# Kernel tuning notes

Measured on AMD Instinct MI355X. Metric: run time of the kernel, lower is better.

## Reference

```python
import jax, jax.numpy as jnp
import numpy as np

TAU = 2.0  # LIF membrane time constant (tau=2.0)
V_TH = 1.0  # spiking threshold (spikingjelly default)

@jax.custom_vjp
def spike(v):
    # Heaviside spike at v >= 0 (input is v - V_TH)
    return (v >= 0.0).astype(v.dtype)

def _spike_fwd(v):
    return spike(v), v

def _spike_bwd(v, g):
    # ATan surrogate gradient (spikingjelly default, alpha=2):
    # d/dv = alpha / (2 * (1 + (pi/2 * alpha * v)^2)) = 1 / (1 + (pi*v)^2)
    return (g / (1.0 + (jnp.pi * v) ** 2),)

spike.defvjp(_spike_fwd, _spike_bwd)

def lif_linear(x, w):
    """SpikLinearLayer: Linear (no bias) then multi-step LIF over leading T axis.
    x: [T, B, N, Din], w: [Dout, Din] -> spikes [T, B, N, Dout]
    LIF: v <- v + (y - v)/tau ; s = H(v - vth) ; hard reset v <- v*(1-s)
    """
    y = jnp.einsum('tbnd,ed->tbne', x, w)
    def step(v, yt):
        v = v + (yt - v) / TAU
        s = spike(v - V_TH)
        return v * (1.0 - s), s
    _, spikes = jax.lax.scan(step, jnp.zeros_like(y[0]), y)
    return spikes

def setup_inputs() -> dict:
    key = jax.random.key(0)
    k0, k1, k2, k3 = jax.random.split(key, 4)
    T, B, N, D, L = 4, 32, 1024, 256, 2
    x = jax.random.normal(k0, (T, B, N, D), dtype=jnp.float32)
    w_in = jax.random.normal(k1, (2 * D, D), dtype=jnp.float32) * 0.05
    w_hidden = jax.random.normal(k2, (L, 2 * D, 2 * D), dtype=jnp.float32) * 0.05
    w_out = jax.random.normal(k3, (D, 2 * D), dtype=jnp.float32) * 0.05
    return {"x": x, "w_in": w_in, "w_hidden": w_hidden, "w_out": w_out}

def reference(x, w_in, w_hidden, w_out):
    # TemporalBlock.forward
    h = lif_linear(x, w_in)                       # [T,B,N,2D]
    for l in range(w_hidden.shape[0]):
        h = h * (1.0 - lif_linear(h, w_hidden[l]))  # multiplicative spike gate
    return lif_linear(h, w_out)                   # [T,B,N,D]
```

## Files before the change

### kernel.cpp

```cpp
#include <hip/hip_runtime.h>
#include <stdint.h>

typedef __attribute__((ext_vector_type(8))) short short8;
typedef __attribute__((ext_vector_type(4))) float f32x4;

constexpr int T_ = 4;
constexpr int BNTOT = 32768;

__device__ __forceinline__ uint32_t bf1(float f) {
    uint32_t x = __builtin_bit_cast(uint32_t, f);
    return (x + 0x7FFFu + ((x >> 16) & 1u)) >> 16;
}
__device__ __forceinline__ uint32_t pk(float lo, float hi) {
    return bf1(lo) | (bf1(hi) << 16);
}

__global__ __launch_bounds__(256)
void cvt_tiled(const float* __restrict__ in, ushort* __restrict__ out) {
    const int g   = blockIdx.x * 256 + threadIdx.x;
    const int kg  = g & 31;
    const int r   = (g >> 5) & 15;
    const int bt  = g >> 9;
    const float* src = in + ((size_t)(bt * 16 + r)) * 256 + kg * 8;
    const float4 a = *(const float4*)src;
    const float4 b = *(const float4*)(src + 4);
    uint4 o;
    o.x = pk(a.x, a.y); o.y = pk(a.z, a.w);
    o.z = pk(b.x, b.y); o.w = pk(b.z, b.w);
    *(uint4*)(out + ((size_t)(bt * 32 + kg)) * 128 + r * 8) = o;
}

template <int MODE, int K, int NOUT>
__global__ __launch_bounds__(256, 3)
void lif_mfma(const ushort* __restrict__ A,
              const float* __restrict__ W,
              void* __restrict__ Out)
{
    __shared__ __align__(16) char smem[8192 + 32768];

    constexpr int NS = K / 32;
    constexpr int NCOLT = NOUT / 64;

    const int tid = threadIdx.x;
    const int l   = tid & 63;
    const int w   = tid >> 6;

    const int id  = blockIdx.x;
    const int xcd = id & 7;
    const int j_  = id >> 3;
    const int row0 = (xcd * 64 + j_ / NCOLT) * 64;
    const int col0 = (j_ % NCOLT) * 64;

    const int rby = (l & 15) * 64;
    const int gp  = ((l >> 4) ^ ((l >> 1) & 3)) << 4;

    const ushort* abase = A +
        ((size_t)(w * (BNTOT / 16) + (row0 >> 4)) * (K / 8) + (l >> 4)) * 128 +
        (l & 15) * 8;

    const int b_col = tid >> 2;
    const float* w_base = W + (size_t)(col0 + b_col) * K +
                          ((tid & 3) ^ ((tid >> 3) & 3)) * 8;
    const int bwo = b_col * 64 + (tid & 3) * 16;

    f32x4 acc[4][4];
#pragma unroll
    for (int m = 0; m < 4; ++m)
#pragma unroll
        for (int n = 0; n < 4; ++n) acc[m][n] = (f32x4)0.f;

    auto loadA = [&](int s, short8 af[4]) {
#pragma unroll
        for (int m = 0; m < 4; ++m)
            af[m] = *(const short8*)(abase + (size_t)m * (K * 16) + s * 512);
    };
    auto loadB = [&](int s, float4& f0, float4& f1) {
        const float* wp = w_base + s * 32;
        f0 = *(const float4*)wp;
        f1 = *(const float4*)(wp + 4);
    };
    auto writeB = [&](const float4& f0, const float4& f1, char* buf) {
        uint4 o;
        o.x = pk(f0.x, f0.y); o.y = pk(f0.z, f0.w);
        o.z = pk(f1.x, f1.y); o.w = pk(f1.z, f1.w);
        *(uint4*)(buf + bwo) = o;
    };
    auto compute = [&](const short8 af[4], const char* buf) {
        short8 bfr[4];
#pragma unroll
        for (int n = 0; n < 4; ++n)
            bfr[n] = *(const short8*)(buf + n * 1024 + rby + gp);
#pragma unroll
        for (int m = 0; m < 4; ++m)
#pragma unroll
            for (int n = 0; n < 4; ++n)
                acc[m][n] = __builtin_amdgcn_mfma_f32_16x16x32_bf16(
                    af[m], bfr[n], acc[m][n], 0, 0, 0);
    };

    char* const bs0 = smem;
    char* const bs1 = smem + 4096;

    short8 aEv[4], aOd[4];
    float4 bEv0, bEv1, bOd0, bOd1;

    loadA(0, aEv);
    loadB(0, bEv0, bEv1);
    writeB(bEv0, bEv1, bs0);
    asm volatile("s_waitcnt lgkmcnt(0)\n\ts_barrier" ::: "memory");

    for (int s = 0; s < NS; s += 2) {
        const int s1 = (s + 1 < NS) ? s + 1 : s;
        loadA(s1, aOd);
        loadB(s1, bOd0, bOd1);
        compute(aEv, bs0);
        writeB(bOd0, bOd1, bs1);
        asm volatile("s_waitcnt lgkmcnt(0)\n\ts_barrier" ::: "memory");

        const int s2 = (s + 2 < NS) ? s + 2 : s;
        loadA(s2, aEv);
        loadB(s2, bEv0, bEv1);
        compute(aOd, bs1);
        writeB(bEv0, bEv1, bs0);
        asm volatile("s_waitcnt lgkmcnt(0)\n\ts_barrier" ::: "memory");
    }

    float* Y = (float*)(smem + 8192);
#pragma unroll
    for (int half = 0; half < 2; ++half) {
#pragma unroll
        for (int nn = 0; nn < 2; ++nn) {
            const int n = half * 2 + nn;
#pragma unroll
            for (int m = 0; m < 4; ++m)
#pragma unroll
                for (int j = 0; j < 4; ++j) {
                    const int row = m * 16 + (l >> 4) * 4 + j;
                    const int cl  = nn * 16 + (l & 15);
                    const int colp = cl ^ (((row >> 2) & 1) << 4);
                    Y[w * 2048 + row * 32 + colp] = acc[m][n][j];
                }
        }
        __syncthreads();
#pragma unroll
        for (int u4 = 0; u4 < 4; ++u4) {
            const int u   = u4 * 256 + tid;
            const int row = u >> 4;
            const int cp  = (u & 15) * 2;
            const int colp = cp ^ (((row >> 2) & 1) << 4);
            float v0 = 0.f, v1 = 0.f;
#pragma unroll
            for (int t = 0; t < T_; ++t) {
                const float2 y = *(const float2*)&Y[t * 2048 + row * 32 + colp];
                v0 = 0.5f * (v0 + y.x);
                v1 = 0.5f * (v1 + y.y);
                const bool s0 = (v0 >= 1.f), s1 = (v1 >= 1.f);
                v0 = s0 ? 0.f : v0;
                v1 = s1 ? 0.f : v1;
                const int grow = row0 + row;
                const int c    = col0 + half * 32 + cp;
                if (MODE == 2) {
                    float2 o;
                    o.x = s0 ? 1.f : 0.f;
                    o.y = s1 ? 1.f : 0.f;
                    *(float2*)((float*)Out + ((size_t)(t * BNTOT + grow)) * NOUT + c) = o;
                } else {
                    const size_t tb = ((size_t)(t * (BNTOT / 16) + (grow >> 4)) *
                                       (NOUT / 8) + (c >> 3)) * 128 + (grow & 15) * 8 + (c & 7);
                    if (MODE == 0) {
                        uint32_t uo = (s0 ? 0x3F80u : 0u) | (s1 ? 0x3F800000u : 0u);
                        *(uint32_t*)((ushort*)Out + tb) = uo;
                    } else {
                        const uint32_t h = *(const uint32_t*)(A + tb);
                        const uint32_t msk = (s0 ? 0u : 0xFFFFu) | (s1 ? 0u : 0xFFFF0000u);
                        *(uint32_t*)((ushort*)Out + tb) = h & msk;
                    }
                }
            }
        }
        __syncthreads();
    }
}

extern "C" void kernel_launch(void* const* d_in, const int* in_sizes, int n_in,
                              void* d_out, int out_size, void* d_ws, size_t ws_size,
                              hipStream_t stream)
{
    const float* x     = (const float*)d_in[0];
    const float* w_in  = (const float*)d_in[1];
    const float* w_h   = (const float*)d_in[2];
    const float* w_out = (const float*)d_in[3];

    ushort* xbf = (ushort*)d_out;
    ushort* hA  = (ushort*)d_ws;
    ushort* hB  = (ushort*)d_out;
    float*  out = (float*)d_out;

    cvt_tiled<<<16384, 256, 0, stream>>>(x, xbf);

    lif_mfma<0, 256, 512><<<8 * 512, 256, 0, stream>>>(xbf, w_in, hA);
    lif_mfma<1, 512, 512><<<8 * 512, 256, 0, stream>>>(hA, w_h, hB);
    lif_mfma<1, 512, 512><<<8 * 512, 256, 0, stream>>>(hB, w_h + 512 * 512, hA);
    lif_mfma<2, 512, 256><<<4 * 512, 256, 0, stream>>>(hA, w_out, out);
}
```

Before: 409.5 us.

## Store spike activations as bytes, preload whole weight slab, fuse T into MFMA tile

Intermediate spike/gated activations are now stored as uint8 0/1 masks instead of bf16 and expanded to bf16 in registers with byte permutes and a multiply. This halves activation traffic between layers. The whole 64-column weight slab is converted into shared memory once per block, replacing the double-buffered per-step pipeline. Each wave now owns 16 rows across all four timesteps, so the LIF recurrence runs directly on accumulator registers without a shared-memory transpose. Risks: occupancy drops to 2 waves per SIMD and shared memory grows to 64KB for K=512. The byte-mask format is exact here only because the gated activations are always 0 or 1.

```diff
diff --git a/kernel.cpp b/kernel.cpp
--- a/kernel.cpp
+++ b/kernel.cpp
@@ -15,12 +15,21 @@
     return bf1(lo) | (bf1(hi) << 16);
 }
 
+__device__ __forceinline__ short8 expand8(uint2 r) {
+    uint4 o;
+    o.x = __builtin_amdgcn_perm(0u, r.x, 0x0C010C00u) * 0x3F80u;
+    o.y = __builtin_amdgcn_perm(0u, r.x, 0x0C030C02u) * 0x3F80u;
+    o.z = __builtin_amdgcn_perm(0u, r.y, 0x0C010C00u) * 0x3F80u;
+    o.w = __builtin_amdgcn_perm(0u, r.y, 0x0C030C02u) * 0x3F80u;
+    return __builtin_bit_cast(short8, o);
+}
+
 __global__ __launch_bounds__(256)
 void cvt_tiled(const float* __restrict__ in, ushort* __restrict__ out) {
-    const int g   = blockIdx.x * 256 + threadIdx.x;
-    const int kg  = g & 31;
-    const int r   = (g >> 5) & 15;
-    const int bt  = g >> 9;
+    const int g  = blockIdx.x * 256 + threadIdx.x;
+    const int kg = g & 31;
+    const int r  = (g >> 5) & 15;
+    const int bt = g >> 9;
     const float* src = in + ((size_t)(bt * 16 + r)) * 256 + kg * 8;
     const float4 a = *(const float4*)src;
     const float4 b = *(const float4*)(src + 4);
@@ -31,15 +40,15 @@
 }
 
 template <int MODE, int K, int NOUT>
-__global__ __launch_bounds__(256, 3)
-void lif_mfma(const ushort* __restrict__ A,
+__global__ __launch_bounds__(256, 2)
+void lif_mfma(const void* __restrict__ Av,
               const float* __restrict__ W,
               void* __restrict__ Out)
 {
-    __shared__ __align__(16) char smem[8192 + 32768];
-
     constexpr int NS = K / 32;
+    constexpr int KG = K / 8;
     constexpr int NCOLT = NOUT / 64;
+    __shared__ __align__(16) char smem[NS * 4096];
 
     const int tid = threadIdx.x;
     const int l   = tid & 63;
@@ -51,134 +60,128 @@
     const int row0 = (xcd * 64 + j_ / NCOLT) * 64;
     const int col0 = (j_ % NCOLT) * 64;
 
-    const int rby = (l & 15) * 64;
-    const int gp  = ((l >> 4) ^ ((l >> 1) & 3)) << 4;
-
-    const ushort* abase = A +
-        ((size_t)(w * (BNTOT / 16) + (row0 >> 4)) * (K / 8) + (l >> 4)) * 128 +
-        (l & 15) * 8;
-
-    const int b_col = tid >> 2;
-    const float* w_base = W + (size_t)(col0 + b_col) * K +
-                          ((tid & 3) ^ ((tid >> 3) & 3)) * 8;
-    const int bwo = b_col * 64 + (tid & 3) * 16;
-
-    f32x4 acc[4][4];
-#pragma unroll
-    for (int m = 0; m < 4; ++m)
-#pragma unroll
-        for (int n = 0; n < 4; ++n) acc[m][n] = (f32x4)0.f;
-
-    auto loadA = [&](int s, short8 af[4]) {
-#pragma unroll
-        for (int m = 0; m < 4; ++m)
-            af[m] = *(const short8*)(abase + (size_t)m * (K * 16) + s * 512);
-    };
-    auto loadB = [&](int s, float4& f0, float4& f1) {
-        const float* wp = w_base + s * 32;
-        f0 = *(const float4*)wp;
-        f1 = *(const float4*)(wp + 4);
-    };
-    auto writeB = [&](const float4& f0, const float4& f1, char* buf) {
-        uint4 o;
-        o.x = pk(f0.x, f0.y); o.y = pk(f0.z, f0.w);
-        o.z = pk(f1.x, f1.y); o.w = pk(f1.z, f1.w);
-        *(uint4*)(buf + bwo) = o;
-    };
-    auto compute = [&](const short8 af[4], const char* buf) {
+    {
+        constexpr int ITERS = 64 * KG / 256;
+#pragma unroll
+        for (int i = 0; i < ITERS; ++i) {
+            const int idx = i * 256 + tid;
+            const int c   = idx / KG;
+            const int kg  = idx % KG;
+            const float* wp = W + (size_t)(col0 + c) * K + kg * 8;
+            const float4 f0 = *(const float4*)wp;
+            const float4 f1 = *(const float4*)(wp + 4);
+            uint4 o;
+            o.x = pk(f0.x, f0.y); o.y = pk(f0.z, f0.w);
+            o.z = pk(f1.x, f1.y); o.w = pk(f1.z, f1.w);
+            const int s = kg >> 2, g = kg & 3;
+            *(uint4*)(smem + ((c >> 4) * NS + s) * 1024 + (c & 15) * 64 +
+                      ((g ^ ((c >> 1) & 3)) * 16)) = o;
+        }
+    }
+    __syncthreads();
+
+    const char* bbase = smem + (l & 15) * 64 + (((l >> 4) ^ ((l >> 1) & 3)) * 16);
+    const int rb = (row0 >> 4) + w;
+
+    f32x4 acc[T_][4];
+#pragma unroll
+    for (int t = 0; t < T_; ++t)
+#pragma unroll
+        for (int n = 0; n < 4; ++n) acc[t][n] = (f32x4)0.f;
+
+    size_t aunit[T_];
+#pragma unroll
+    for (int t = 0; t < T_; ++t)
+        aunit[t] = ((size_t)(t * (BNTOT / 16) + rb)) * KG + (l >> 4);
+
+    auto loadAb = [&](int s, short8 a[T_]) {
+#pragma unroll
+        for (int t = 0; t < T_; ++t)
+            a[t] = *(const short8*)((const ushort*)Av +
+                     (aunit[t] + s * 4) * 128 + (l & 15) * 8);
+    };
+    auto loadAu = [&](int s, uint2 a[T_]) {
+#pragma unroll
+        for (int t = 0; t < T_; ++t)
+            a[t] = *(const uint2*)((const uint8_t*)Av +
+                     (aunit[t] + s * 4) * 128 + (l & 15) * 8);
+    };
+    auto stepB = [&](const short8 a[T_], int s) {
         short8 bfr[4];
 #pragma unroll
         for (int n = 0; n < 4; ++n)
-            bfr[n] = *(const short8*)(buf + n * 1024 + rby + gp);
-#pragma unroll
-        for (int m = 0; m < 4; ++m)
+            bfr[n] = *(const short8*)(bbase + (n * NS + s) * 1024);
+#pragma unroll
+        for (int t = 0; t < T_; ++t)
 #pragma unroll
             for (int n = 0; n < 4; ++n)
-                acc[m][n] = __builtin_amdgcn_mfma_f32_16x16x32_bf16(
-                    af[m], bfr[n], acc[m][n], 0, 0, 0);
-    };
-
-    char* const bs0 = smem;
-    char* const bs1 = smem + 4096;
-
-    short8 aEv[4], aOd[4];
-    float4 bEv0, bEv1, bOd0, bOd1;
-
-    loadA(0, aEv);
-    loadB(0, bEv0, bEv1);
-    writeB(bEv0, bEv1, bs0);
-    asm volatile("s_waitcnt lgkmcnt(0)\n\ts_barrier" ::: "memory");
-
-    for (int s = 0; s < NS; s += 2) {
-        const int s1 = (s + 1 < NS) ? s + 1 : s;
-        loadA(s1, aOd);
-        loadB(s1, bOd0, bOd1);
-        compute(aEv, bs0);
-        writeB(bOd0, bOd1, bs1);
-        asm volatile("s_waitcnt lgkmcnt(0)\n\ts_barrier" ::: "memory");
-
-        const int s2 = (s + 2 < NS) ? s + 2 : s;
-        loadA(s2, aEv);
-        loadB(s2, bEv0, bEv1);
-        compute(aOd, bs1);
-        writeB(bEv0, bEv1, bs0);
-        asm volatile("s_waitcnt lgkmcnt(0)\n\ts_barrier" ::: "memory");
+                acc[t][n] = __builtin_amdgcn_mfma_f32_16x16x32_bf16(
+                    a[t], bfr[n], acc[t][n], 0, 0, 0);
+    };
+    auto stepU = [&](const uint2 a[T_], int s) {
+        short8 bfr[4];
+#pragma unroll
+        for (int n = 0; n < 4; ++n)
+            bfr[n] = *(const short8*)(bbase + (n * NS + s) * 1024);
+#pragma unroll
+        for (int t = 0; t < T_; ++t) {
+            const short8 af = expand8(a[t]);
+#pragma unroll
+            for (int n = 0; n < 4; ++n)
+                acc[t][n] = __builtin_amdgcn_mfma_f32_16x16x32_bf16(
+                    af, bfr[n], acc[t][n], 0, 0, 0);
+        }
+    };
+
+    if constexpr (MODE == 0) {
+        short8 a0[T_], a1[T_];
+        loadAb(0, a0);
+        for (int s = 0; s < NS; s += 2) {
+            loadAb(s + 1, a1);
+            stepB(a0, s);
+            loadAb(s + 2 < NS ? s + 2 : 0, a0);
+            stepB(a1, s + 1);
+        }
+    } else {
+        uint2 a0[T_], a1[T_];
+        loadAu(0, a0);
+        for (int s = 0; s < NS; s += 2) {
+            loadAu(s + 1, a1);
+            stepU(a0, s);
+            loadAu(s + 2 < NS ? s + 2 : 0, a0);
+            stepU(a1, s + 1);
+        }
     }
 
-    float* Y = (float*)(smem + 8192);
-#pragma unroll
-    for (int half = 0; half < 2; ++half) {
-#pragma unroll
-        for (int nn = 0; nn < 2; ++nn) {
-            const int n = half * 2 + nn;
-#pragma unroll
-            for (int m = 0; m < 4; ++m)
-#pragma unroll
-                for (int j = 0; j < 4; ++j) {
-                    const int row = m * 16 + (l >> 4) * 4 + j;
-                    const int cl  = nn * 16 + (l & 15);
-                    const int colp = cl ^ (((row >> 2) & 1) << 4);
-                    Y[w * 2048 + row * 32 + colp] = acc[m][n][j];
-                }
-        }
-        __syncthreads();
-#pragma unroll
-        for (int u4 = 0; u4 < 4; ++u4) {
-            const int u   = u4 * 256 + tid;
-            const int row = u >> 4;
-            const int cp  = (u & 15) * 2;
-            const int colp = cp ^ (((row >> 2) & 1) << 4);
-            float v0 = 0.f, v1 = 0.f;
+#pragma unroll
+    for (int n = 0; n < 4; ++n) {
+#pragma unroll
+        for (int j = 0; j < 4; ++j) {
+            const int rl   = (l >> 4) * 4 + j;
+            const int grow = row0 + w * 16 + rl;
+            const int c    = col0 + n * 16 + (l & 15);
+            float v = 0.f;
 #pragma unroll
             for (int t = 0; t < T_; ++t) {
-                const float2 y = *(const float2*)&Y[t * 2048 + row * 32 + colp];
-                v0 = 0.5f * (v0 + y.x);
-                v1 = 0.5f * (v1 + y.y);
-                const bool s0 = (v0 >= 1.f), s1 = (v1 >= 1.f);
-                v0 = s0 ? 0.f : v0;
-                v1 = s1 ? 0.f : v1;
-                const int grow = row0 + row;
-                const int c    = col0 + half * 32 + cp;
-                if (MODE == 2) {
-                    float2 o;
-                    o.x = s0 ? 1.f : 0.f;
-                    o.y = s1 ? 1.f : 0.f;
-                    *(float2*)((float*)Out + ((size_t)(t * BNTOT + grow)) * NOUT + c) = o;
+                v = 0.5f * (v + acc[t][n][j]);
+                const bool sp = (v >= 1.f);
+                if (sp) v = 0.f;
+                if constexpr (MODE == 2) {
+                    ((float*)Out)[((size_t)(t * BNTOT + grow)) * NOUT + c] =
+                        sp ? 1.f : 0.f;
                 } else {
-                    const size_t tb = ((size_t)(t * (BNTOT / 16) + (grow >> 4)) *
-                                       (NOUT / 8) + (c >> 3)) * 128 + (grow & 15) * 8 + (c & 7);
-                    if (MODE == 0) {
-                        uint32_t uo = (s0 ? 0x3F80u : 0u) | (s1 ? 0x3F800000u : 0u);
-                        *(uint32_t*)((ushort*)Out + tb) = uo;
+                    const size_t tb =
+                        ((size_t)(t * (BNTOT / 16) + (grow >> 4)) * (NOUT / 8) +
+                         (c >> 3)) * 128 + rl * 8 + (c & 7);
+                    if constexpr (MODE == 0) {
+                        ((uint8_t*)Out)[tb] = sp ? 1 : 0;
                     } else {
-                        const uint32_t h = *(const uint32_t*)(A + tb);
-                        const uint32_t msk = (s0 ? 0u : 0xFFFFu) | (s1 ? 0u : 0xFFFF0000u);
-                        *(uint32_t*)((ushort*)Out + tb) = h & msk;
+                        const uint8_t h = ((const uint8_t*)Av)[tb];
+                        ((uint8_t*)Out)[tb] = sp ? 0 : h;
                     }
                 }
             }
         }
-        __syncthreads();
     }
 }
 
@@ -191,15 +194,15 @@
     const float* w_h   = (const float*)d_in[2];
     const float* w_out = (const float*)d_in[3];
 
-    ushort* xbf = (ushort*)d_out;
-    ushort* hA  = (ushort*)d_ws;
-    ushort* hB  = (ushort*)d_out;
-    float*  out = (float*)d_out;
+    ushort*  xbf = (ushort*)d_out;
+    uint8_t* hA  = (uint8_t*)d_ws;
+    uint8_t* hB  = hA + (size_t)T_ * BNTOT * 512;
+    float*   out = (float*)d_out;
 
     cvt_tiled<<<16384, 256, 0, stream>>>(x, xbf);
 
-    lif_mfma<0, 256, 512><<<8 * 512, 256, 0, stream>>>(xbf, w_in, hA);
-    lif_mfma<1, 512, 512><<<8 * 512, 256, 0, stream>>>(hA, w_h, hB);
-    lif_mfma<1, 512, 512><<<8 * 512, 256, 0, stream>>>(hB, w_h + 512 * 512, hA);
-    lif_mfma<2, 512, 256><<<4 * 512, 256, 0, stream>>>(hA, w_out, out);
-}
+    lif_mfma<0, 256, 512><<<4096, 256, 0, stream>>>(xbf, w_in, hA);
+    lif_mfma<1, 512, 512><<<4096, 256, 0, stream>>>(hA, w_h, hB);
+    lif_mfma<1, 512, 512><<<4096, 256, 0, stream>>>(hB, w_h + 512 * 512, hA);
+    lif_mfma<2, 512, 256><<<2048, 256, 0, stream>>>(hA, w_out, out);
+}
```

New measurement: 348.7 us. -14.9%, faster.
